# Kernel optimization log

Hardware: AMD Instinct MI355X
Metric: run time of the kernel (lower is better)

## Reference

```python
import jax, jax.numpy as jnp
import numpy as np

EMB = 1024
N_HEADS = 16
HEAD = EMB // N_HEADS
EPS = 1e-5


def layernorm(x, g, b):
    mu = jnp.mean(x, axis=-1, keepdims=True)
    var = jnp.var(x, axis=-1, keepdims=True)
    return (x - mu) * jax.lax.rsqrt(var + EPS) * g + b


def setup_inputs() -> dict:
    key = jax.random.key(0)
    ks = jax.random.split(key, 12)
    s = lambda fan_in: 1.0 / np.sqrt(fan_in)
    return {
        "x": jax.random.normal(ks[0], (8, 1024, EMB), dtype=jnp.float32),
        "ln1_g": jnp.ones((EMB,), jnp.float32),
        "ln1_b": jnp.zeros((EMB,), jnp.float32),
        "wq": jax.random.uniform(ks[1], (EMB, EMB), jnp.float32, -s(EMB), s(EMB)),
        "wk": jax.random.uniform(ks[2], (EMB, EMB), jnp.float32, -s(EMB), s(EMB)),
        "wv": jax.random.uniform(ks[3], (EMB, EMB), jnp.float32, -s(EMB), s(EMB)),
        "w_proj": jax.random.uniform(ks[4], (EMB, EMB), jnp.float32, -s(EMB), s(EMB)),
        "b_proj": jnp.zeros((EMB,), jnp.float32),
        "ln2_g": jnp.ones((EMB,), jnp.float32),
        "ln2_b": jnp.zeros((EMB,), jnp.float32),
        "w1": jax.random.uniform(ks[5], (EMB, 4 * EMB), jnp.float32, -s(EMB), s(EMB)),
        "b1": jnp.zeros((4 * EMB,), jnp.float32),
        "w2": jax.random.uniform(ks[6], (4 * EMB, EMB), jnp.float32, -s(4 * EMB), s(4 * EMB)),
        "b2": jnp.zeros((EMB,), jnp.float32),
    }


def reference(x, ln1_g, ln1_b, wq, wk, wv, w_proj, b_proj, ln2_g, ln2_b, w1, b1, w2, b2):
    B, T, E = x.shape
    h = layernorm(x, ln1_g, ln1_b)
    # per-head no-bias projections == one big matmul then split into heads
    q = (h @ wq).reshape(B, T, N_HEADS, HEAD).transpose(0, 2, 1, 3)  # [B,H,T,D]
    k = (h @ wk).reshape(B, T, N_HEADS, HEAD).transpose(0, 2, 1, 3)
    v = (h @ wv).reshape(B, T, N_HEADS, HEAD).transpose(0, 2, 1, 3)
    scores = jnp.einsum("bhqd,bhkd->bhqk", q, k) * (HEAD ** -0.5)
    causal = jnp.tril(jnp.ones((T, T), dtype=bool))
    scores = jnp.where(causal, scores, -jnp.inf)
    wei = jax.nn.softmax(scores, axis=-1)  # dropout is identity at eval
    attn = jnp.einsum("bhqk,bhkd->bhqd", wei, v)
    attn = attn.transpose(0, 2, 1, 3).reshape(B, T, E)
    out = x + attn @ w_proj + b_proj
    h2 = layernorm(out, ln2_g, ln2_b)
    mlp = jax.nn.gelu(h2 @ w1 + b1, approximate=False) @ w2 + b2
    return out + mlp
```

## Files before the change

kernel.cpp:

```cpp
#include <hip/hip_runtime.h>
#include <hip/hip_bf16.h>

#define EMB 1024
#define NH 16
#define HD 64
#define BATCH 8
#define SEQ 1024
#define ROWS (BATCH*SEQ)
#define MT (ROWS/128)

typedef unsigned short ushort_t;
typedef __attribute__((ext_vector_type(8))) short bf16x8;
typedef __attribute__((ext_vector_type(4))) float f32x4;
typedef __attribute__((ext_vector_type(16))) float f32x16;

__device__ __forceinline__ float bf2f(ushort_t u){
    union { unsigned int i; float f; } v; v.i = ((unsigned int)u) << 16; return v.f;
}
__device__ __forceinline__ ushort_t f2bf(float f){
    unsigned int u = __float_as_uint(f);
    unsigned int r = (u + 0x7FFFu + ((u >> 16) & 1u)) >> 16;
    return (ushort_t)r;
}
__device__ __forceinline__ void gload16(const ushort_t* g, ushort_t* l){
    __builtin_amdgcn_global_load_lds(
        (const __attribute__((address_space(1))) void*)g,
        (__attribute__((address_space(3))) void*)l,
        16, 0, 0);
}
__device__ __forceinline__ float gelu_f(float v){
    float x = fabsf(v) * 0.70710678118654752f;
    float t = __builtin_amdgcn_rcpf(1.0f + 0.3275911f * x);
    float poly = t*(0.254829592f + t*(-0.284496736f + t*(1.421413741f + t*(-1.453152027f + t*1.061405429f))));
    float erfa = 1.0f - poly * __expf(-x*x);
    float erfv = (v >= 0.f) ? erfa : -erfa;
    return 0.5f * v * (1.0f + erfv);
}

__global__ __launch_bounds__(256) void prep_kernel(const float* __restrict__ x,
                                                   const float* __restrict__ ln1_g,
                                                   const float* __restrict__ ln1_b,
                                                   ushort_t* __restrict__ h1,
                                                   const float* __restrict__ wq,
                                                   const float* __restrict__ wk,
                                                   const float* __restrict__ wv,
                                                   const float* __restrict__ w_proj,
                                                   const float* __restrict__ w1,
                                                   const float* __restrict__ w2,
                                                   ushort_t* __restrict__ wqkv_t,
                                                   ushort_t* __restrict__ wproj_t,
                                                   ushort_t* __restrict__ w1_t,
                                                   ushort_t* __restrict__ w2_t){
    int bid = blockIdx.x;
    int tid = threadIdx.x;
    if (bid < ROWS){
        __shared__ float ss[4], qq[4];
        __shared__ float mu_s, sc_s;
        const float* xr = x + (size_t)bid * EMB;
        float4 f = *(const float4*)(xr + tid*4);
        float v[4] = {f.x, f.y, f.z, f.w};
        float s = v[0]+v[1]+v[2]+v[3];
        float q = v[0]*v[0]+v[1]*v[1]+v[2]*v[2]+v[3]*v[3];
        #pragma unroll
        for (int o = 32; o > 0; o >>= 1){ s += __shfl_down(s, o); q += __shfl_down(q, o); }
        int wave = tid >> 6, lane = tid & 63;
        if (lane == 0){ ss[wave] = s; qq[wave] = q; }
        __syncthreads();
        if (tid == 0){
            float S = ss[0]+ss[1]+ss[2]+ss[3];
            float Q = qq[0]+qq[1]+qq[2]+qq[3];
            float mu = S * (1.0f/EMB);
            float var = Q * (1.0f/EMB) - mu*mu;
            mu_s = mu; sc_s = rsqrtf(var + 1e-5f);
        }
        __syncthreads();
        float mu = mu_s, sc = sc_s;
        float4 gu = *(const float4*)(ln1_g + tid*4);
        float4 bu = *(const float4*)(ln1_b + tid*4);
        ushort4 o4;
        o4.x = f2bf((v[0]-mu)*sc*gu.x + bu.x);
        o4.y = f2bf((v[1]-mu)*sc*gu.y + bu.y);
        o4.z = f2bf((v[2]-mu)*sc*gu.z + bu.z);
        o4.w = f2bf((v[3]-mu)*sc*gu.w + bu.w);
        *(ushort4*)(h1 + (size_t)bid*EMB + tid*4) = o4;
    } else {
        __shared__ ushort_t t[32][33];
        int j = bid - ROWS;
        const float* in; ushort_t* out; int K, N, bx, by;
        if (j < 3072){
            int which = j >> 10, jj = j & 1023;
            in = (which == 0) ? wq : (which == 1) ? wk : wv;
            out = wqkv_t + (size_t)which * 1024 * 1024;
            K = 1024; N = 1024; bx = jj & 31; by = jj >> 5;
        } else if (j < 4096){
            int jj = j - 3072;
            in = w_proj; out = wproj_t; K = 1024; N = 1024; bx = jj & 31; by = jj >> 5;
        } else if (j < 8192){
            int jj = j - 4096;
            in = w1; out = w1_t; K = 1024; N = 4096; bx = jj & 127; by = jj >> 7;
        } else {
            int jj = j - 8192;
            in = w2; out = w2_t; K = 4096; N = 1024; bx = jj & 31; by = jj >> 5;
        }
        int tx = tid & 31, ty = tid >> 5;
        #pragma unroll
        for (int r = 0; r < 4; ++r)
            t[ty + r*8][tx] = f2bf(in[(size_t)(by*32 + ty + r*8) * N + bx*32 + tx]);
        __syncthreads();
        #pragma unroll
        for (int r = 0; r < 4; ++r)
            out[(size_t)(bx*32 + ty + r*8) * K + by*32 + tx] = t[tx][ty + r*8];
    }
}

__global__ __launch_bounds__(256) void ln_kernel(const float* __restrict__ xin,
                                                 const float* __restrict__ g,
                                                 const float* __restrict__ bia,
                                                 ushort_t* __restrict__ out){
    int row = blockIdx.x;
    int tid = threadIdx.x;
    const float* x = xin + (size_t)row * EMB;
    float4 f = *(const float4*)(x + tid*4);
    float v[4] = {f.x, f.y, f.z, f.w};
    float s = v[0]+v[1]+v[2]+v[3];
    float q = v[0]*v[0]+v[1]*v[1]+v[2]*v[2]+v[3]*v[3];
    #pragma unroll
    for (int o = 32; o > 0; o >>= 1){ s += __shfl_down(s, o); q += __shfl_down(q, o); }
    __shared__ float ss[4], qq[4];
    __shared__ float mu_s, sc_s;
    int wave = tid >> 6, lane = tid & 63;
    if (lane == 0){ ss[wave] = s; qq[wave] = q; }
    __syncthreads();
    if (tid == 0){
        float S = ss[0]+ss[1]+ss[2]+ss[3];
        float Q = qq[0]+qq[1]+qq[2]+qq[3];
        float mu = S * (1.0f/EMB);
        float var = Q * (1.0f/EMB) - mu*mu;
        mu_s = mu; sc_s = rsqrtf(var + 1e-5f);
    }
    __syncthreads();
    float mu = mu_s, sc = sc_s;
    float4 gu = *(const float4*)(g + tid*4);
    float4 bu = *(const float4*)(bia + tid*4);
    ushort4 o4;
    o4.x = f2bf((v[0]-mu)*sc*gu.x + bu.x);
    o4.y = f2bf((v[1]-mu)*sc*gu.y + bu.y);
    o4.z = f2bf((v[2]-mu)*sc*gu.z + bu.z);
    o4.w = f2bf((v[3]-mu)*sc*gu.w + bu.w);
    *(ushort4*)(out + (size_t)row*EMB + tid*4) = o4;
}

template<int MODE>
__global__ __launch_bounds__(256) void gemm_kernel(const ushort_t* __restrict__ A,
                                                   const ushort_t* __restrict__ Bt,
                                                   const float* __restrict__ bias,
                                                   const float* __restrict__ resid,
                                                   void* __restrict__ out,
                                                   int M, int N, int K){
    __shared__ ushort_t As[128*64];
    __shared__ ushort_t Bs[128*64];
    int tid = threadIdx.x;
    int lane = tid & 63, wave = tid >> 6;
    int l31 = lane & 31, half = lane >> 5;
    int wm = wave >> 1, wn = wave & 1;
    int bid = blockIdx.x;
    int m0 = (bid & (MT-1)) * 128, n0 = (bid >> 6) * 128;

    f32x16 acc[2][2];
    #pragma unroll
    for (int i=0;i<2;i++)
        #pragma unroll
        for (int j=0;j<2;j++)
            #pragma unroll
            for (int r=0;r<16;r++) acc[i][j][r] = 0.f;

    int lr  = lane >> 3;
    int lch = lane & 7;
    const ushort_t* gA = A  + (size_t)(m0 + wave*32 + lr)*K + (lch ^ lr)*8;
    const ushort_t* gB = Bt + (size_t)(n0 + wave*32 + lr)*K + (lch ^ lr)*8;
    ushort_t* lA = &As[(wave*32)*64];
    ushort_t* lB = &Bs[(wave*32)*64];
    int sx = lane & 7;

    for (int k0 = 0; k0 < K; k0 += 64){
        #pragma unroll
        for (int i = 0; i < 4; ++i){
            gload16(gA + (size_t)(i*8)*K + k0, lA + i*8*64);
            gload16(gB + (size_t)(i*8)*K + k0, lB + i*8*64);
        }
        __syncthreads();
        #pragma unroll
        for (int s = 0; s < 4; ++s){
            int ch = ((s<<1) | half) ^ sx;
            bf16x8 af[2], bfr[2];
            #pragma unroll
            for (int i=0;i<2;i++) af[i]  = *(const bf16x8*)&As[(wm*64 + i*32 + l31)*64 + ch*8];
            #pragma unroll
            for (int j=0;j<2;j++) bfr[j] = *(const bf16x8*)&Bs[(wn*64 + j*32 + l31)*64 + ch*8];
            #pragma unroll
            for (int i=0;i<2;i++)
                #pragma unroll
                for (int j=0;j<2;j++)
                    acc[i][j] = __builtin_amdgcn_mfma_f32_32x32x16_bf16(af[i], bfr[j], acc[i][j], 0,0,0);
        }
        __syncthreads();
    }

    int rowoff = 4*half;
    #pragma unroll
    for (int i=0;i<2;i++){
        #pragma unroll
        for (int j=0;j<2;j++){
            int n = n0 + wn*64 + j*32 + l31;
            #pragma unroll
            for (int reg=0; reg<16; ++reg){
                int m = m0 + wm*64 + i*32 + (reg&3) + 8*(reg>>2) + rowoff;
                float v = acc[i][j][reg];
                size_t idx = (size_t)m*N + n;
                if (MODE == 0){
                    ((ushort_t*)out)[idx] = f2bf(v);
                } else if (MODE == 1){
                    v += bias[n] + resid[idx];
                    ((float*)out)[idx] = v;
                } else if (MODE == 2){
                    v += bias[n];
                    ((ushort_t*)out)[idx] = f2bf(gelu_f(v));
                } else {
                    v += bias[n] + resid[idx];
                    ((float*)out)[idx] = v;
                }
            }
        }
    }
}

__global__ __launch_bounds__(256) void attn_kernel(const ushort_t* __restrict__ qkv,
                                                   ushort_t* __restrict__ attn_out){
    __shared__ ushort_t Qs[128*64];
    __shared__ ushort_t Ks[64*64];
    __shared__ ushort_t Vts[64][72];
    __shared__ ushort_t Ps[128*64];

    int tid = threadIdx.x;
    int lane = tid & 63, wave = tid >> 6;
    int quad = lane >> 4, l15 = lane & 15;
    int pair = blockIdx.x;
    int bh = blockIdx.y;
    int b = bh >> 4, h = bh & 15;
    size_t tb = (size_t)b * SEQ;

    int lr = lane >> 3, lch = lane & 7;
    int tr = tid >> 3;
    int tc = (tid & 7) * 8;
    int sw_w = tid & 7;
    int sx = l15 & 7;

    for (int t = 0; t < 2; ++t){
        int qi = t ? (7 - pair) : pair;

        {
            const ushort_t* gq = qkv + (size_t)(tb + qi*128 + wave*32 + lr)*3072 + h*64 + (lch^lr)*8;
            ushort_t* lq = &Qs[(wave*32)*64];
            #pragma unroll
            for (int p = 0; p < 4; ++p)
                gload16(gq + (size_t)(p*8)*3072, lq + p*8*64);
        }

        f32x4 o_acc[4][2];
        #pragma unroll
        for (int i=0;i<4;i++)
            #pragma unroll
            for (int j=0;j<2;j++) o_acc[i][j] = (f32x4){0.f,0.f,0.f,0.f};
        float m_st[2] = {-1e30f, -1e30f};
        float l_st[2] = {0.f, 0.f};

        int nj = 2*qi + 2;
        for (int j = 0; j < nj; ++j){
            {
                const ushort_t* gk = qkv + (size_t)(tb + j*64 + wave*16 + lr)*3072 + 1024 + h*64 + (lch^lr)*8;
                ushort_t* lk = &Ks[(wave*16)*64];
                gload16(gk, lk);
                gload16(gk + (size_t)8*3072, lk + 8*64);
            }
            #pragma unroll
            for (int p = 0; p < 2; ++p){
                int r = tr + p*32;
                bf16x8 vv = *(const bf16x8*)(qkv + (size_t)(tb + j*64 + r)*3072 + 2048 + h*64 + tc);
                int kcol = r ^ (sw_w << 3);
                #pragma unroll
                for (int c = 0; c < 8; ++c) Vts[tc + c][kcol] = (ushort_t)vv[c];
            }
            __syncthreads();

            f32x4 st[4][2];
            #pragma unroll
            for (int mt=0;mt<4;mt++)
                #pragma unroll
                for (int nt=0;nt<2;nt++) st[mt][nt] = (f32x4){0.f,0.f,0.f,0.f};
            #pragma unroll
            for (int kf = 0; kf < 2; ++kf){
                int ch = (kf*4 + quad) ^ sx;
                bf16x8 ak[4], bq[2];
                #pragma unroll
                for (int mt=0;mt<4;mt++) ak[mt] = *(const bf16x8*)&Ks[(mt*16 + l15)*64 + ch*8];
                #pragma unroll
                for (int nt=0;nt<2;nt++) bq[nt] = *(const bf16x8*)&Qs[(wave*32 + nt*16 + l15)*64 + ch*8];
                #pragma unroll
                for (int mt=0;mt<4;mt++)
                    #pragma unroll
                    for (int nt=0;nt<2;nt++)
                        st[mt][nt] = __builtin_amdgcn_mfma_f32_16x16x32_bf16(ak[mt], bq[nt], st[mt][nt], 0,0,0);
            }

            bool need_mask = (j >= 2*qi);
            #pragma unroll
            for (int mt=0;mt<4;mt++)
                #pragma unroll
                for (int nt=0;nt<2;nt++)
                    #pragma unroll
                    for (int r=0;r<4;r++){
                        float s = st[mt][nt][r] * 0.125f;
                        if (need_mask){
                            int kg = j*64 + mt*16 + quad*4 + r;
                            int qg = qi*128 + wave*32 + nt*16 + l15;
                            if (kg > qg) s = -1e30f;
                        }
                        st[mt][nt][r] = s;
                    }

            #pragma unroll
            for (int nt = 0; nt < 2; ++nt){
                float mx = st[0][nt][0];
                #pragma unroll
                for (int mt=0;mt<4;mt++)
                    #pragma unroll
                    for (int r=0;r<4;r++) mx = fmaxf(mx, st[mt][nt][r]);
                mx = fmaxf(mx, __shfl_xor(mx, 16));
                mx = fmaxf(mx, __shfl_xor(mx, 32));
                float mnew = fmaxf(m_st[nt], mx);
                float al = __expf(m_st[nt] - mnew);
                float ps = 0.f;
                #pragma unroll
                for (int mt=0;mt<4;mt++)
                    #pragma unroll
                    for (int r=0;r<4;r++){
                        float p = __expf(st[mt][nt][r] - mnew);
                        st[mt][nt][r] = p;
                        ps += p;
                    }
                ps += __shfl_xor(ps, 16);
                ps += __shfl_xor(ps, 32);
                l_st[nt] = l_st[nt]*al + ps;
                m_st[nt] = mnew;
                #pragma unroll
                for (int mtd=0;mtd<4;mtd++)
                    #pragma unroll
                    for (int r=0;r<4;r++) o_acc[mtd][nt][r] *= al;
                #pragma unroll
                for (int mt=0;mt<4;mt++){
                    int slot = (mt*2 + (quad>>1)) ^ sx;
                    ushort4 pk;
                    pk.x = f2bf(st[mt][nt][0]); pk.y = f2bf(st[mt][nt][1]);
                    pk.z = f2bf(st[mt][nt][2]); pk.w = f2bf(st[mt][nt][3]);
                    *(ushort4*)&Ps[(wave*32 + nt*16 + l15)*64 + slot*8 + (quad&1)*4] = pk;
                }
            }

            #pragma unroll
            for (int kf = 0; kf < 2; ++kf){
                bf16x8 av[4], bp[2];
                #pragma unroll
                for (int mtd=0;mtd<4;mtd++){
                    int d = mtd*16 + l15;
                    int col = (kf*32 + quad*8) ^ (((d >> 3) & 7) << 3);
                    av[mtd] = *(const bf16x8*)&Vts[d][col];
                }
                #pragma unroll
                for (int nt=0;nt<2;nt++){
                    int ch = (kf*4 + quad) ^ sx;
                    bp[nt] = *(const bf16x8*)&Ps[(wave*32 + nt*16 + l15)*64 + ch*8];
                }
                #pragma unroll
                for (int mtd=0;mtd<4;mtd++)
                    #pragma unroll
                    for (int nt=0;nt<2;nt++)
                        o_acc[mtd][nt] = __builtin_amdgcn_mfma_f32_16x16x32_bf16(av[mtd], bp[nt], o_acc[mtd][nt], 0,0,0);
            }
            __syncthreads();
        }

        #pragma unroll
        for (int nt = 0; nt < 2; ++nt){
            float inv = 1.0f / l_st[nt];
            size_t tok = tb + qi*128 + wave*32 + nt*16 + l15;
            #pragma unroll
            for (int mtd = 0; mtd < 4; ++mtd){
                ushort4 ok;
                ok.x = f2bf(o_acc[mtd][nt][0]*inv); ok.y = f2bf(o_acc[mtd][nt][1]*inv);
                ok.z = f2bf(o_acc[mtd][nt][2]*inv); ok.w = f2bf(o_acc[mtd][nt][3]*inv);
                *(ushort4*)(attn_out + tok*EMB + h*64 + mtd*16 + quad*4) = ok;
            }
        }
    }
}

extern "C" void kernel_launch(void* const* d_in, const int* in_sizes, int n_in,
                              void* d_out, int out_size, void* d_ws, size_t ws_size,
                              hipStream_t stream){
    const float* x      = (const float*)d_in[0];
    const float* ln1_g  = (const float*)d_in[1];
    const float* ln1_b  = (const float*)d_in[2];
    const float* wq     = (const float*)d_in[3];
    const float* wk     = (const float*)d_in[4];
    const float* wv     = (const float*)d_in[5];
    const float* w_proj = (const float*)d_in[6];
    const float* b_proj = (const float*)d_in[7];
    const float* ln2_g  = (const float*)d_in[8];
    const float* ln2_b  = (const float*)d_in[9];
    const float* w1     = (const float*)d_in[10];
    const float* b1     = (const float*)d_in[11];
    const float* w2     = (const float*)d_in[12];
    const float* b2     = (const float*)d_in[13];
    float* outp = (float*)d_out;

    char* ws = (char*)d_ws;
    size_t off = 0;
    auto alloc = [&](size_t bytes)->char*{ char* p = ws + off; off += (bytes + 255) & ~255ULL; return p; };
    ushort_t* wqkv_t = (ushort_t*)alloc((size_t)3072*1024*2);
    ushort_t* wproj_t= (ushort_t*)alloc((size_t)1024*1024*2);
    ushort_t* w1_t   = (ushort_t*)alloc((size_t)4096*1024*2);
    ushort_t* w2_t   = (ushort_t*)alloc((size_t)1024*4096*2);
    ushort_t* qkv    = (ushort_t*)alloc((size_t)ROWS*3072*2);
    ushort_t* hbuf   = (ushort_t*)alloc((size_t)ROWS*1024*2);
    float*    out32  = (float*)  alloc((size_t)ROWS*1024*4);
    ushort_t* mid    = (ushort_t*)alloc((size_t)ROWS*4096*2);
    ushort_t* h1 = hbuf;
    ushort_t* attn = hbuf;
    ushort_t* h2 = qkv;

    dim3 blk(256);
    prep_kernel<<<dim3(20480), blk, 0, stream>>>(x, ln1_g, ln1_b, h1,
                                                 wq, wk, wv, w_proj, w1, w2,
                                                 wqkv_t, wproj_t, w1_t, w2_t);
    gemm_kernel<0><<<dim3(MT*(3072/128)), blk, 0, stream>>>(h1, wqkv_t, nullptr, nullptr, qkv, ROWS, 3072, 1024);
    attn_kernel<<<dim3(4,128), blk, 0, stream>>>(qkv, attn);
    gemm_kernel<1><<<dim3(MT*(1024/128)), blk, 0, stream>>>(attn, wproj_t, b_proj, x, out32, ROWS, 1024, 1024);
    ln_kernel<<<ROWS, blk, 0, stream>>>(out32, ln2_g, ln2_b, h2);
    gemm_kernel<2><<<dim3(MT*(4096/128)), blk, 0, stream>>>(h2, w1_t, b1, nullptr, mid, ROWS, 4096, 1024);
    gemm_kernel<3><<<dim3(MT*(1024/128)), blk, 0, stream>>>(mid, w2_t, b2, out32, outp, ROWS, 1024, 4096);
}
```

Baseline: 462.0 us.

## Double-buffer GEMM LDS tiles and enlarge block tile to 256x128 with 8 waves

The GEMM kernel now uses 512 threads per block with a 256x128 output tile and double-buffered LDS, so the next K-slice loads asynchronously while MFMAs run on the current one. The two barriers per K step become a single vmcnt-wait plus barrier. Each wave computes a 128x32 sub-tile, reusing one B fragment across four A fragments. This raises LDS use to 96KB per block and register pressure, and halves the number of blocks, which may cut occupancy and the number of blocks available to fill the GPU.

```diff
diff --git a/kernel.cpp b/kernel.cpp
--- a/kernel.cpp
+++ b/kernel.cpp
@@ -7,7 +7,6 @@
 #define BATCH 8
 #define SEQ 1024
 #define ROWS (BATCH*SEQ)
-#define MT (ROWS/128)
 
 typedef unsigned short ushort_t;
 typedef __attribute__((ext_vector_type(8))) short bf16x8;
@@ -27,6 +26,11 @@
         (const __attribute__((address_space(1))) void*)g,
         (__attribute__((address_space(3))) void*)l,
         16, 0, 0);
+}
+__device__ __forceinline__ void tile_sync(){
+    asm volatile("s_waitcnt vmcnt(0)" ::: "memory");
+    __builtin_amdgcn_s_barrier();
+    asm volatile("" ::: "memory");
 }
 __device__ __forceinline__ float gelu_f(float v){
     float x = fabsf(v) * 0.70710678118654752f;
@@ -151,84 +155,82 @@
 }
 
 template<int MODE>
-__global__ __launch_bounds__(256) void gemm_kernel(const ushort_t* __restrict__ A,
-                                                   const ushort_t* __restrict__ Bt,
-                                                   const float* __restrict__ bias,
-                                                   const float* __restrict__ resid,
-                                                   void* __restrict__ out,
-                                                   int M, int N, int K){
-    __shared__ ushort_t As[128*64];
-    __shared__ ushort_t Bs[128*64];
+__global__ __launch_bounds__(512, 2) void gemm_kernel(const ushort_t* __restrict__ A,
+                                                      const ushort_t* __restrict__ Bt,
+                                                      const float* __restrict__ bias,
+                                                      const float* __restrict__ resid,
+                                                      void* __restrict__ out,
+                                                      int M, int N, int K){
+    __shared__ ushort_t As[2][256*64];
+    __shared__ ushort_t Bs[2][128*64];
     int tid = threadIdx.x;
     int lane = tid & 63, wave = tid >> 6;
     int l31 = lane & 31, half = lane >> 5;
-    int wm = wave >> 1, wn = wave & 1;
+    int wm = wave >> 2, wn = wave & 3;
     int bid = blockIdx.x;
-    int m0 = (bid & (MT-1)) * 128, n0 = (bid >> 6) * 128;
-
-    f32x16 acc[2][2];
+    int m0 = (bid & 31) * 256, n0 = (bid >> 5) * 128;
+
+    f32x16 acc[4];
     #pragma unroll
-    for (int i=0;i<2;i++)
-        #pragma unroll
-        for (int j=0;j<2;j++)
-            #pragma unroll
-            for (int r=0;r<16;r++) acc[i][j][r] = 0.f;
+    for (int i=0;i<4;i++)
+        #pragma unroll
+        for (int r=0;r<16;r++) acc[i][r] = 0.f;
 
     int lr  = lane >> 3;
     int lch = lane & 7;
     const ushort_t* gA = A  + (size_t)(m0 + wave*32 + lr)*K + (lch ^ lr)*8;
-    const ushort_t* gB = Bt + (size_t)(n0 + wave*32 + lr)*K + (lch ^ lr)*8;
-    ushort_t* lA = &As[(wave*32)*64];
-    ushort_t* lB = &Bs[(wave*32)*64];
+    const ushort_t* gB = Bt + (size_t)(n0 + wave*16 + lr)*K + (lch ^ lr)*8;
     int sx = lane & 7;
-
-    for (int k0 = 0; k0 < K; k0 += 64){
-        #pragma unroll
-        for (int i = 0; i < 4; ++i){
-            gload16(gA + (size_t)(i*8)*K + k0, lA + i*8*64);
-            gload16(gB + (size_t)(i*8)*K + k0, lB + i*8*64);
-        }
-        __syncthreads();
+    int NT = K >> 6;
+
+    auto stage = [&](int b, int k0){
+        ushort_t* lA = &As[b][(wave*32)*64];
+        ushort_t* lB = &Bs[b][(wave*16)*64];
+        #pragma unroll
+        for (int i = 0; i < 4; ++i) gload16(gA + (size_t)(i*8)*K + k0, lA + i*8*64);
+        #pragma unroll
+        for (int p = 0; p < 2; ++p) gload16(gB + (size_t)(p*8)*K + k0, lB + p*8*64);
+    };
+
+    stage(0, 0);
+    tile_sync();
+    int cur = 0;
+    for (int t = 0; t < NT; ++t){
+        if (t + 1 < NT) stage(cur ^ 1, (t + 1) << 6);
+        const ushort_t* Ac = As[cur];
+        const ushort_t* Bc = Bs[cur];
         #pragma unroll
         for (int s = 0; s < 4; ++s){
             int ch = ((s<<1) | half) ^ sx;
-            bf16x8 af[2], bfr[2];
-            #pragma unroll
-            for (int i=0;i<2;i++) af[i]  = *(const bf16x8*)&As[(wm*64 + i*32 + l31)*64 + ch*8];
-            #pragma unroll
-            for (int j=0;j<2;j++) bfr[j] = *(const bf16x8*)&Bs[(wn*64 + j*32 + l31)*64 + ch*8];
-            #pragma unroll
-            for (int i=0;i<2;i++)
-                #pragma unroll
-                for (int j=0;j<2;j++)
-                    acc[i][j] = __builtin_amdgcn_mfma_f32_32x32x16_bf16(af[i], bfr[j], acc[i][j], 0,0,0);
-        }
-        __syncthreads();
+            bf16x8 af[4];
+            #pragma unroll
+            for (int i=0;i<4;i++) af[i] = *(const bf16x8*)&Ac[(wm*128 + i*32 + l31)*64 + ch*8];
+            bf16x8 bfr = *(const bf16x8*)&Bc[(wn*32 + l31)*64 + ch*8];
+            #pragma unroll
+            for (int i=0;i<4;i++)
+                acc[i] = __builtin_amdgcn_mfma_f32_32x32x16_bf16(af[i], bfr, acc[i], 0,0,0);
+        }
+        if (t + 1 < NT) tile_sync();
+        cur ^= 1;
     }
 
+    int n = n0 + wn*32 + l31;
+    float bn = (MODE != 0) ? bias[n] : 0.f;
     int rowoff = 4*half;
     #pragma unroll
-    for (int i=0;i<2;i++){
-        #pragma unroll
-        for (int j=0;j<2;j++){
-            int n = n0 + wn*64 + j*32 + l31;
-            #pragma unroll
-            for (int reg=0; reg<16; ++reg){
-                int m = m0 + wm*64 + i*32 + (reg&3) + 8*(reg>>2) + rowoff;
-                float v = acc[i][j][reg];
-                size_t idx = (size_t)m*N + n;
-                if (MODE == 0){
-                    ((ushort_t*)out)[idx] = f2bf(v);
-                } else if (MODE == 1){
-                    v += bias[n] + resid[idx];
-                    ((float*)out)[idx] = v;
-                } else if (MODE == 2){
-                    v += bias[n];
-                    ((ushort_t*)out)[idx] = f2bf(gelu_f(v));
-                } else {
-                    v += bias[n] + resid[idx];
-                    ((float*)out)[idx] = v;
-                }
+    for (int i=0;i<4;i++){
+        #pragma unroll
+        for (int reg=0; reg<16; ++reg){
+            int m = m0 + wm*128 + i*32 + (reg&3) + 8*(reg>>2) + rowoff;
+            float v = acc[i][reg];
+            size_t idx = (size_t)m*N + n;
+            if (MODE == 0){
+                ((ushort_t*)out)[idx] = f2bf(v);
+            } else if (MODE == 1 || MODE == 3){
+                v += bn + resid[idx];
+                ((float*)out)[idx] = v;
+            } else {
+                ((ushort_t*)out)[idx] = f2bf(gelu_f(v + bn));
             }
         }
     }
@@ -439,13 +441,14 @@
     ushort_t* h2 = qkv;
 
     dim3 blk(256);
+    dim3 gblk(512);
     prep_kernel<<<dim3(20480), blk, 0, stream>>>(x, ln1_g, ln1_b, h1,
                                                  wq, wk, wv, w_proj, w1, w2,
                                                  wqkv_t, wproj_t, w1_t, w2_t);
-    gemm_kernel<0><<<dim3(MT*(3072/128)), blk, 0, stream>>>(h1, wqkv_t, nullptr, nullptr, qkv, ROWS, 3072, 1024);
+    gemm_kernel<0><<<dim3(32*(3072/128)), gblk, 0, stream>>>(h1, wqkv_t, nullptr, nullptr, qkv, ROWS, 3072, 1024);
     attn_kernel<<<dim3(4,128), blk, 0, stream>>>(qkv, attn);
-    gemm_kernel<1><<<dim3(MT*(1024/128)), blk, 0, stream>>>(attn, wproj_t, b_proj, x, out32, ROWS, 1024, 1024);
+    gemm_kernel<1><<<dim3(32*(1024/128)), gblk, 0, stream>>>(attn, wproj_t, b_proj, x, out32, ROWS, 1024, 1024);
     ln_kernel<<<ROWS, blk, 0, stream>>>(out32, ln2_g, ln2_b, h2);
-    gemm_kernel<2><<<dim3(MT*(4096/128)), blk, 0, stream>>>(h2, w1_t, b1, nullptr, mid, ROWS, 4096, 1024);
-    gemm_kernel<3><<<dim3(MT*(1024/128)), blk, 0, stream>>>(mid, w2_t, b2, out32, outp, ROWS, 1024, 4096);
-}
+    gemm_kernel<2><<<dim3(32*(4096/128)), gblk, 0, stream>>>(h2, w1_t, b1, nullptr, mid, ROWS, 4096, 1024);
+    gemm_kernel<3><<<dim3(32*(1024/128)), gblk, 0, stream>>>(mid, w2_t, b2, out32, outp, ROWS, 1024, 4096);
+}
```

Measured after the change: 509.9 us. +10.4%, slower.
